# Optimization experiments

Measured on AMD Instinct MI355X. Metric: run time of the kernel, lower is better.

## Reference

```python
import jax, jax.numpy as jnp
import numpy as np

NEI_SIZE = [16]  # matches init kwarg nei_size

def setup_inputs() -> dict:
    key = jax.random.key(0)
    k = jax.random.split(key, 5)
    B, N, S = 512, 32, 16
    EF, NF = 64, 128
    return {
        "x": jax.random.normal(k[0], (B, N, NF), dtype=jnp.float32),
        "x_nei_rel": jax.random.normal(k[1], (B, N * S, EF), dtype=jnp.float32),
        "x_nei_node": jax.random.normal(k[2], (B, N * S, NF), dtype=jnp.float32),
        "W1_w": jax.random.normal(k[3], (NF, EF + NF), dtype=jnp.float32) * 0.05,
        "W1_b": jax.random.normal(k[4], (NF,), dtype=jnp.float32) * 0.05,
        "i": 0,
    }

def reference(x, x_nei_rel, x_nei_node, W1_w, W1_b, i):
    S = NEI_SIZE[i]                       # now_nei_size (static python int)
    B, N, D = x.shape                     # N = n_neibor, D = nodeFea
    norm = 1.0 / np.sqrt(D).astype(np.float32)
    # concat edge+node feats and project: [B, N*S, EF+NF] -> [B, N*S, D]
    x_nei = jnp.concatenate([x_nei_rel, x_nei_node], axis=-1)
    v = (x_nei @ W1_w.T + W1_b).reshape(B, N, S, D)
    # per-node attention over its S neighbors
    alpha = jnp.einsum('bnd,bnsd->bns', x, v) * norm   # [B, N, S]
    alpha = jax.nn.softmax(alpha, axis=-1)
    # weighted neighbor sum
    return jnp.einsum('bns,bnsd->bnd', alpha, v)       # [B, N, D]
```

## Files before the change

### kernel.cpp

```cpp
#include <hip/hip_runtime.h>
#include <stdint.h>


typedef __attribute__((ext_vector_type(8))) short short8;
typedef __attribute__((ext_vector_type(4))) float float4_t;
typedef __attribute__((ext_vector_type(4))) unsigned short ushort4_t;

#define GRID_ 1024
#define ITERS_ 8

__device__ __forceinline__ unsigned short f2bf(float f) {
    uint32_t u = __float_as_uint(f);
    u += 0x7fffu + ((u >> 16) & 1u);
    return (unsigned short)(u >> 16);
}

__device__ __forceinline__ int aoff(int s, int kc) {
    int X = ((kc >> 5) << 6) + (((kc & 31) >> 3) << 4) + s;
    X ^= ((X >> 3) ^ (X >> 6)) & 7;
    return X * 8 + (kc & 7);
}

__global__ __launch_bounds__(512, 8) void nei_attn_kernel(
    const float* __restrict__ x,
    const float* __restrict__ rel,
    const float* __restrict__ node,
    const float* __restrict__ W,
    const float* __restrict__ bias,
    float* __restrict__ out)
{
    __shared__ __align__(16) unsigned short lds_a[2][6 * 64 * 8];
    __shared__ float lds_x[2][128];
    __shared__ float lds_v[2][16 * 132];
    __shared__ float lds_alpha[2][16];

    const int t    = threadIdx.x;
    const int tl   = t & 255;
    const int h    = t >> 8;
    const int lane = t & 63;
    const int wv   = t >> 6;
    const int l15  = lane & 15;
    const int quad = (lane >> 4) & 3;

    short8 bf[6];
    const int row = wv * 16 + l15;
    const float bias_c = bias[row];
    #pragma unroll
    for (int q = 0; q < 6; ++q) {
        const float* p = W + row * 192 + q * 32 + quad * 8;
        float4_t a0 = *(const float4_t*)p;
        float4_t a1 = *(const float4_t*)(p + 4);
        short8 f;
        f[0] = (short)f2bf(a0.x); f[1] = (short)f2bf(a0.y);
        f[2] = (short)f2bf(a0.z); f[3] = (short)f2bf(a0.w);
        f[4] = (short)f2bf(a1.x); f[5] = (short)f2bf(a1.y);
        f[6] = (short)f2bf(a1.z); f[7] = (short)f2bf(a1.w);
        bf[q] = f;
    }

    const int s0 = tl >> 4,  kc0 = (tl & 15) << 2;
    const int s1 = tl >> 5,  kc1 = 64 + ((tl & 31) << 2);
    const int s2 = s1 + 8;
    const int ao0 = h * 3072 + aoff(s0, kc0);
    const int ao1 = h * 3072 + aoff(s1, kc1);
    const int ao2 = h * 3072 + aoff(s2, kc1);
    const int lx = lane ^ ((lane >> 3) & 7);
    unsigned short* la = &lds_a[0][0];

    int idx = blockIdx.x * (ITERS_ * 2);

    #pragma unroll 1
    for (int it = 0; it < ITERS_; ++it) {
        {
            const float* pr = rel  + (idx + h) * 1024;
            const float* pn = node + (idx + h) * 2048;
            float4_t pf0 = *(const float4_t*)(pr + tl * 4);
            float4_t pf1 = *(const float4_t*)(pn + tl * 4);
            float4_t pf2 = *(const float4_t*)(pn + 1024 + tl * 4);
            ushort4_t u;
            u[0] = f2bf(pf0.x); u[1] = f2bf(pf0.y); u[2] = f2bf(pf0.z); u[3] = f2bf(pf0.w);
            *(ushort4_t*)&la[ao0] = u;
            u[0] = f2bf(pf1.x); u[1] = f2bf(pf1.y); u[2] = f2bf(pf1.z); u[3] = f2bf(pf1.w);
            *(ushort4_t*)&la[ao1] = u;
            u[0] = f2bf(pf2.x); u[1] = f2bf(pf2.y); u[2] = f2bf(pf2.z); u[3] = f2bf(pf2.w);
            *(ushort4_t*)&la[ao2] = u;
            if (t < 256) lds_x[t >> 7][t & 127] = x[(idx + (t >> 7)) * 128 + (t & 127)];
        }
        __syncthreads();

        float4_t acc0 = {0.f, 0.f, 0.f, 0.f};
        float4_t acc1 = {0.f, 0.f, 0.f, 0.f};
        #pragma unroll
        for (int q = 0; q < 6; ++q) {
            short8 af0 = *(const short8*)&la[(q * 64 + (lx ^ q)) * 8];
            short8 af1 = *(const short8*)&la[3072 + (q * 64 + (lx ^ q)) * 8];
            acc0 = __builtin_amdgcn_mfma_f32_16x16x32_bf16(af0, bf[q], acc0, 0, 0, 0);
            acc1 = __builtin_amdgcn_mfma_f32_16x16x32_bf16(af1, bf[q], acc1, 0, 0, 0);
        }
        const int colw = wv * 16 + l15;
        const int rb = quad * 4;
        #pragma unroll
        for (int r = 0; r < 4; ++r) {
            lds_v[0][(rb + r) * 132 + colw] = acc0[r] + bias_c;
            lds_v[1][(rb + r) * 132 + colw] = acc1[r] + bias_c;
        }
        __syncthreads();

        {
            const int sA = tl >> 4, dA = tl & 15;
            const float* vx = &lds_x[h][dA * 8];
            const float* vv = &lds_v[h][sA * 132 + dA * 8];
            float p = 0.f;
            #pragma unroll
            for (int j = 0; j < 8; ++j) p += vx[j] * vv[j];
            p += __shfl_xor(p, 8);
            p += __shfl_xor(p, 4);
            p += __shfl_xor(p, 2);
            p += __shfl_xor(p, 1);
            if (dA == 0) lds_alpha[h][sA] = p * 0.08838834764831845f;
        }
        __syncthreads();

        if (tl < 128) {
            const float* al = lds_alpha[h];
            float m = al[0];
            #pragma unroll
            for (int s = 1; s < 16; ++s) m = fmaxf(m, al[s]);
            float den = 0.f, o = 0.f;
            #pragma unroll
            for (int s = 0; s < 16; ++s) {
                const float e = __expf(al[s] - m);
                den += e;
                o += e * lds_v[h][s * 132 + tl];
            }
            out[(idx + h) * 128 + tl] = o / den;
        }
        idx += 2;
    }
}

extern "C" void kernel_launch(void* const* d_in, const int* in_sizes, int n_in,
                              void* d_out, int out_size, void* d_ws, size_t ws_size,
                              hipStream_t stream) {
    const float* x    = (const float*)d_in[0];
    const float* rel  = (const float*)d_in[1];
    const float* node = (const float*)d_in[2];
    const float* W    = (const float*)d_in[3];
    const float* bias = (const float*)d_in[4];
    float* out = (float*)d_out;
    hipLaunchKernelGGL(nei_attn_kernel, dim3(GRID_), dim3(512), 0, stream,
                       x, rel, node, W, bias, out);
}
```

Measured before the change: 285.8 us.

## Give each wave its own node tile with W in LDS and register-level softmax

Work moves from block-level cooperation on two nodes per iteration to each wave processing its own node tiles. W is converted to bf16 once into shared memory, and the node's neighbor features are loaded straight from global memory into MFMA A-fragments in registers. The next tile is prefetched while the current one is computed. The attention dot product, softmax and weighted sum are all done with cross-lane shuffles, which removes every per-iteration __syncthreads and LDS round trip. In exchange, each wave re-reads 48 W fragments from LDS per tile, register pressure rises (launch bounds 256,3), and the global loads are less coalesced.

```diff
diff --git a/kernel.cpp b/kernel.cpp
--- a/kernel.cpp
+++ b/kernel.cpp
@@ -7,7 +7,7 @@
 typedef __attribute__((ext_vector_type(4))) unsigned short ushort4_t;
 
 #define GRID_ 1024
-#define ITERS_ 8
+#define TPW_  4
 
 __device__ __forceinline__ unsigned short f2bf(float f) {
     uint32_t u = __float_as_uint(f);
@@ -15,13 +15,7 @@
     return (unsigned short)(u >> 16);
 }
 
-__device__ __forceinline__ int aoff(int s, int kc) {
-    int X = ((kc >> 5) << 6) + (((kc & 31) >> 3) << 4) + s;
-    X ^= ((X >> 3) ^ (X >> 6)) & 7;
-    return X * 8 + (kc & 7);
-}
-
-__global__ __launch_bounds__(512, 8) void nei_attn_kernel(
+__global__ __launch_bounds__(256, 3) void nei_attn_kernel(
     const float* __restrict__ x,
     const float* __restrict__ rel,
     const float* __restrict__ node,
@@ -29,114 +23,148 @@
     const float* __restrict__ bias,
     float* __restrict__ out)
 {
-    __shared__ __align__(16) unsigned short lds_a[2][6 * 64 * 8];
-    __shared__ float lds_x[2][128];
-    __shared__ float lds_v[2][16 * 132];
-    __shared__ float lds_alpha[2][16];
+    __shared__ __align__(16) unsigned short lds_w[3072 * 8];
 
     const int t    = threadIdx.x;
-    const int tl   = t & 255;
-    const int h    = t >> 8;
     const int lane = t & 63;
     const int wv   = t >> 6;
-    const int l15  = lane & 15;
-    const int quad = (lane >> 4) & 3;
+    const int c    = lane & 15;
+    const int quad = lane >> 4;
 
-    short8 bf[6];
-    const int row = wv * 16 + l15;
-    const float bias_c = bias[row];
     #pragma unroll
-    for (int q = 0; q < 6; ++q) {
-        const float* p = W + row * 192 + q * 32 + quad * 8;
-        float4_t a0 = *(const float4_t*)p;
-        float4_t a1 = *(const float4_t*)(p + 4);
-        short8 f;
-        f[0] = (short)f2bf(a0.x); f[1] = (short)f2bf(a0.y);
-        f[2] = (short)f2bf(a0.z); f[3] = (short)f2bf(a0.w);
-        f[4] = (short)f2bf(a1.x); f[5] = (short)f2bf(a1.y);
-        f[6] = (short)f2bf(a1.z); f[7] = (short)f2bf(a1.w);
-        bf[q] = f;
+    for (int i = 0; i < 12; ++i) {
+        const int slot = t + i * 256;
+        const int ct  = slot / 384;
+        const int rem = slot - ct * 384;
+        const int q   = rem >> 6;
+        const int l   = rem & 63;
+        const int row = ct * 16 + (l & 15);
+        const int kb  = q * 32 + (l >> 4) * 8;
+        const float* wp = W + row * 192 + kb;
+        float4_t w0 = *(const float4_t*)wp;
+        float4_t w1 = *(const float4_t*)(wp + 4);
+        ushort4_t u0, u1;
+        u0[0] = f2bf(w0.x); u0[1] = f2bf(w0.y); u0[2] = f2bf(w0.z); u0[3] = f2bf(w0.w);
+        u1[0] = f2bf(w1.x); u1[1] = f2bf(w1.y); u1[2] = f2bf(w1.z); u1[3] = f2bf(w1.w);
+        *(ushort4_t*)&lds_w[slot * 8]     = u0;
+        *(ushort4_t*)&lds_w[slot * 8 + 4] = u1;
     }
 
-    const int s0 = tl >> 4,  kc0 = (tl & 15) << 2;
-    const int s1 = tl >> 5,  kc1 = 64 + ((tl & 31) << 2);
-    const int s2 = s1 + 8;
-    const int ao0 = h * 3072 + aoff(s0, kc0);
-    const int ao1 = h * 3072 + aoff(s1, kc1);
-    const int ao2 = h * 3072 + aoff(s2, kc1);
-    const int lx = lane ^ ((lane >> 3) & 7);
-    unsigned short* la = &lds_a[0][0];
+    float bv[8];
+    #pragma unroll
+    for (int ct = 0; ct < 8; ++ct) bv[ct] = bias[ct * 16 + c];
 
-    int idx = blockIdx.x * (ITERS_ * 2);
+    __syncthreads();
+
+    int idx = (blockIdx.x * 4 + wv) * TPW_;
+
+    #define LOAD_TILE(BUF, IDX) {                                          \
+        const float* pr = rel  + (IDX) * 1024 + c * 64  + quad * 8;        \
+        const float* pn = node + (IDX) * 2048 + c * 128 + quad * 8;        \
+        BUF[0]  = *(const float4_t*)pr;        BUF[1]  = *(const float4_t*)(pr + 4);   \
+        BUF[2]  = *(const float4_t*)(pr + 32); BUF[3]  = *(const float4_t*)(pr + 36);  \
+        BUF[4]  = *(const float4_t*)pn;        BUF[5]  = *(const float4_t*)(pn + 4);   \
+        BUF[6]  = *(const float4_t*)(pn + 32); BUF[7]  = *(const float4_t*)(pn + 36);  \
+        BUF[8]  = *(const float4_t*)(pn + 64); BUF[9]  = *(const float4_t*)(pn + 68);  \
+        BUF[10] = *(const float4_t*)(pn + 96); BUF[11] = *(const float4_t*)(pn + 100); }
+
+    float4_t buf[12];
+    LOAD_TILE(buf, idx)
 
     #pragma unroll 1
-    for (int it = 0; it < ITERS_; ++it) {
-        {
-            const float* pr = rel  + (idx + h) * 1024;
-            const float* pn = node + (idx + h) * 2048;
-            float4_t pf0 = *(const float4_t*)(pr + tl * 4);
-            float4_t pf1 = *(const float4_t*)(pn + tl * 4);
-            float4_t pf2 = *(const float4_t*)(pn + 1024 + tl * 4);
-            ushort4_t u;
-            u[0] = f2bf(pf0.x); u[1] = f2bf(pf0.y); u[2] = f2bf(pf0.z); u[3] = f2bf(pf0.w);
-            *(ushort4_t*)&la[ao0] = u;
-            u[0] = f2bf(pf1.x); u[1] = f2bf(pf1.y); u[2] = f2bf(pf1.z); u[3] = f2bf(pf1.w);
-            *(ushort4_t*)&la[ao1] = u;
-            u[0] = f2bf(pf2.x); u[1] = f2bf(pf2.y); u[2] = f2bf(pf2.z); u[3] = f2bf(pf2.w);
-            *(ushort4_t*)&la[ao2] = u;
-            if (t < 256) lds_x[t >> 7][t & 127] = x[(idx + (t >> 7)) * 128 + (t & 127)];
-        }
-        __syncthreads();
+    for (int it = 0; it < TPW_; ++it) {
+        float xv[8];
+        #pragma unroll
+        for (int ct = 0; ct < 8; ++ct) xv[ct] = x[idx * 128 + ct * 16 + c];
 
-        float4_t acc0 = {0.f, 0.f, 0.f, 0.f};
-        float4_t acc1 = {0.f, 0.f, 0.f, 0.f};
+        short8 af[6];
         #pragma unroll
         for (int q = 0; q < 6; ++q) {
-            short8 af0 = *(const short8*)&la[(q * 64 + (lx ^ q)) * 8];
-            short8 af1 = *(const short8*)&la[3072 + (q * 64 + (lx ^ q)) * 8];
-            acc0 = __builtin_amdgcn_mfma_f32_16x16x32_bf16(af0, bf[q], acc0, 0, 0, 0);
-            acc1 = __builtin_amdgcn_mfma_f32_16x16x32_bf16(af1, bf[q], acc1, 0, 0, 0);
+            float4_t lo = buf[2 * q], hi = buf[2 * q + 1];
+            short8 f;
+            f[0] = (short)f2bf(lo.x); f[1] = (short)f2bf(lo.y);
+            f[2] = (short)f2bf(lo.z); f[3] = (short)f2bf(lo.w);
+            f[4] = (short)f2bf(hi.x); f[5] = (short)f2bf(hi.y);
+            f[6] = (short)f2bf(hi.z); f[7] = (short)f2bf(hi.w);
+            af[q] = f;
         }
-        const int colw = wv * 16 + l15;
-        const int rb = quad * 4;
+
+        if (it + 1 < TPW_) LOAD_TILE(buf, idx + 1)
+
+        float4_t acc[8];
         #pragma unroll
-        for (int r = 0; r < 4; ++r) {
-            lds_v[0][(rb + r) * 132 + colw] = acc0[r] + bias_c;
-            lds_v[1][(rb + r) * 132 + colw] = acc1[r] + bias_c;
+        for (int ct = 0; ct < 8; ++ct) acc[ct] = (float4_t){0.f, 0.f, 0.f, 0.f};
+        #pragma unroll
+        for (int ct = 0; ct < 8; ++ct) {
+            #pragma unroll
+            for (int q = 0; q < 6; ++q) {
+                short8 wf = *(const short8*)&lds_w[(ct * 6 + q) * 512 + lane * 8];
+                acc[ct] = __builtin_amdgcn_mfma_f32_16x16x32_bf16(af[q], wf, acc[ct], 0, 0, 0);
+            }
         }
-        __syncthreads();
+        #pragma unroll
+        for (int ct = 0; ct < 8; ++ct) {
+            #pragma unroll
+            for (int r = 0; r < 4; ++r) acc[ct][r] += bv[ct];
+        }
 
-        {
-            const int sA = tl >> 4, dA = tl & 15;
-            const float* vx = &lds_x[h][dA * 8];
-            const float* vv = &lds_v[h][sA * 132 + dA * 8];
-            float p = 0.f;
-            #pragma unroll
-            for (int j = 0; j < 8; ++j) p += vx[j] * vv[j];
-            p += __shfl_xor(p, 8);
-            p += __shfl_xor(p, 4);
-            p += __shfl_xor(p, 2);
-            p += __shfl_xor(p, 1);
-            if (dA == 0) lds_alpha[h][sA] = p * 0.08838834764831845f;
+        float p0 = 0.f, p1 = 0.f, p2 = 0.f, p3 = 0.f;
+        #pragma unroll
+        for (int ct = 0; ct < 8; ++ct) {
+            p0 += xv[ct] * acc[ct][0];
+            p1 += xv[ct] * acc[ct][1];
+            p2 += xv[ct] * acc[ct][2];
+            p3 += xv[ct] * acc[ct][3];
         }
-        __syncthreads();
+        #pragma unroll
+        for (int m = 1; m <= 8; m <<= 1) {
+            p0 += __shfl_xor(p0, m);
+            p1 += __shfl_xor(p1, m);
+            p2 += __shfl_xor(p2, m);
+            p3 += __shfl_xor(p3, m);
+        }
+        const float norm = 0.08838834764831845f;
+        p0 *= norm; p1 *= norm; p2 *= norm; p3 *= norm;
+        float q10 = __shfl_xor(p0, 16), q11 = __shfl_xor(p1, 16),
+              q12 = __shfl_xor(p2, 16), q13 = __shfl_xor(p3, 16);
+        float q20 = __shfl_xor(p0, 32), q21 = __shfl_xor(p1, 32),
+              q22 = __shfl_xor(p2, 32), q23 = __shfl_xor(p3, 32);
+        float q30 = __shfl_xor(p0, 48), q31 = __shfl_xor(p1, 48),
+              q32 = __shfl_xor(p2, 48), q33 = __shfl_xor(p3, 48);
 
-        if (tl < 128) {
-            const float* al = lds_alpha[h];
-            float m = al[0];
-            #pragma unroll
-            for (int s = 1; s < 16; ++s) m = fmaxf(m, al[s]);
-            float den = 0.f, o = 0.f;
-            #pragma unroll
-            for (int s = 0; s < 16; ++s) {
-                const float e = __expf(al[s] - m);
-                den += e;
-                o += e * lds_v[h][s * 132 + tl];
-            }
-            out[(idx + h) * 128 + tl] = o / den;
+        float mx = fmaxf(fmaxf(fmaxf(p0, p1), fmaxf(p2, p3)),
+                         fmaxf(fmaxf(fmaxf(q10, q11), fmaxf(q12, q13)),
+                               fmaxf(fmaxf(fmaxf(q20, q21), fmaxf(q22, q23)),
+                                     fmaxf(fmaxf(q30, q31), fmaxf(q32, q33)))));
+        float e0 = __expf(p0 - mx), e1 = __expf(p1 - mx),
+              e2 = __expf(p2 - mx), e3 = __expf(p3 - mx);
+        float den = e0 + e1 + e2 + e3
+                  + __expf(q10 - mx) + __expf(q11 - mx) + __expf(q12 - mx) + __expf(q13 - mx)
+                  + __expf(q20 - mx) + __expf(q21 - mx) + __expf(q22 - mx) + __expf(q23 - mx)
+                  + __expf(q30 - mx) + __expf(q31 - mx) + __expf(q32 - mx) + __expf(q33 - mx);
+        const float inv = 1.0f / den;
+
+        float o[8];
+        #pragma unroll
+        for (int ct = 0; ct < 8; ++ct) {
+            float v = e0 * acc[ct][0] + e1 * acc[ct][1]
+                    + e2 * acc[ct][2] + e3 * acc[ct][3];
+            v += __shfl_xor(v, 16);
+            v += __shfl_xor(v, 32);
+            o[ct] = v;
         }
-        idx += 2;
+
+        float s0 = 0.f, s1 = 0.f;
+        #pragma unroll
+        for (int g = 0; g < 4; ++g) {
+            if (g == quad) { s0 = o[2 * g]; s1 = o[2 * g + 1]; }
+        }
+        out[idx * 128 + quad * 32 + c]      = s0 * inv;
+        out[idx * 128 + quad * 32 + 16 + c] = s1 * inv;
+
+        ++idx;
     }
+    #undef LOAD_TILE
 }
 
 extern "C" void kernel_launch(void* const* d_in, const int* in_sizes, int n_in,
@@ -148,6 +176,6 @@
     const float* W    = (const float*)d_in[3];
     const float* bias = (const float*)d_in[4];
     float* out = (float*)d_out;
-    hipLaunchKernelGGL(nei_attn_kernel, dim3(GRID_), dim3(512), 0, stream,
+    hipLaunchKernelGGL(nei_attn_kernel, dim3(GRID_), dim3(256), 0, stream,
                        x, rel, node, W, bias, out);
 }
```

Result: slower. 385.7 us (+34.9%).
